# Kernel tuning notes

Measured on AMD Instinct MI355X. Metric: run time of the kernel, lower is better.

## Reference

```python
import jax, jax.numpy as jnp
import numpy as np

N, H, DE, E = 100000, 64, 16, 1600000
COORD_SCALE = 0.1


def _lin_params(key, din, dout):
    kw, kb = jax.random.split(key)
    W = jax.random.normal(kw, (din, dout), dtype=jnp.float32) * 0.02
    b = jax.random.normal(kb, (dout,), dtype=jnp.float32) * 0.02
    return W, b


def setup_inputs() -> dict:
    key = jax.random.key(0)
    ks = jax.random.split(key, 10)
    h = jax.random.normal(ks[0], (N, H), dtype=jnp.float32)
    pos = jax.random.normal(ks[1], (N, 3), dtype=jnp.float32)
    edge_index = jax.random.randint(ks[2], (2, E), 0, N, dtype=jnp.int32)
    edge_attr = jax.random.normal(ks[3], (E, DE), dtype=jnp.float32)
    W_e1, b_e1 = _lin_params(ks[4], 2 * H + 1 + DE, H)
    W_e2, b_e2 = _lin_params(ks[5], H, H)
    W_c1, b_c1 = _lin_params(ks[6], H, H)
    W_c2, b_c2 = _lin_params(ks[7], H, 1)
    W_n, b_n = _lin_params(ks[8], 2 * H, H)
    ln_g = jnp.ones((H,), dtype=jnp.float32)
    ln_b = jnp.zeros((H,), dtype=jnp.float32)
    return dict(h=h, pos=pos, edge_index=edge_index, edge_attr=edge_attr,
                W_e1=W_e1, b_e1=b_e1, W_e2=W_e2, b_e2=b_e2,
                W_c1=W_c1, b_c1=b_c1, W_c2=W_c2, b_c2=b_c2,
                W_n=W_n, b_n=b_n, ln_g=ln_g, ln_b=ln_b)


def reference(h, pos, edge_index, edge_attr,
              W_e1, b_e1, W_e2, b_e2,
              W_c1, b_c1, W_c2, b_c2,
              W_n, b_n, ln_g, ln_b):
    src, dst = edge_index[0], edge_index[1]
    pos_src = pos[src]            # [E,3] gather
    pos_dst = pos[dst]
    diff = pos_dst - pos_src      # [E,3]
    dist2 = jnp.clip(jnp.sum(diff * diff, axis=-1, keepdims=True), 0.0, 1000.0)  # [E,1]
    direction = diff / jnp.sqrt(dist2 + 1e-8)

    # edge MLP: phi_e(h_i, h_j, d2, e_ij)
    edge_input = jnp.concatenate([h[src], h[dst], dist2, edge_attr], axis=-1)  # [E, 2H+1+De]
    m = jax.nn.relu(edge_input @ W_e1 + b_e1)
    m_ij = jax.nn.relu(m @ W_e2 + b_e2)  # [E,H]

    # coord MLP -> scalar coef, tanh * scale
    c = jax.nn.relu(m_ij @ W_c1 + b_c1)
    coord_coef = jnp.tanh(c @ W_c2 + b_c2) * COORD_SCALE  # [E,1]
    trans = direction * coord_coef  # [E,3]

    # scatter-add to dst
    delta_pos = jnp.zeros_like(pos).at[dst].add(trans)
    pos_out = pos + delta_pos

    agg_msg = jnp.zeros_like(h).at[dst].add(m_ij)  # [N,H]

    # node MLP + residual + LayerNorm
    h_update = jax.nn.relu(jnp.concatenate([h, agg_msg], axis=-1) @ W_n + b_n)
    x = h + h_update
    mu = jnp.mean(x, axis=-1, keepdims=True)
    var = jnp.mean((x - mu) ** 2, axis=-1, keepdims=True)
    h_out = (x - mu) / jnp.sqrt(var + 1e-5) * ln_g + ln_b
    return h_out, pos_out
```

## Files before the change

kernel.cpp:

```cpp
#include <hip/hip_runtime.h>

using f32x4  = __attribute__((ext_vector_type(4))) float;
using short8 = __attribute__((ext_vector_type(8))) short;

__device__ inline short f2bf(float x) {
    union { float f; unsigned u; } v; v.f = x;
    unsigned r = v.u + 0x7fffu + ((v.u >> 16) & 1u);
    return (short)(r >> 16);
}

__device__ inline short8 pack8(float4 a, float4 b) {
    short8 r;
    r[0] = f2bf(a.x); r[1] = f2bf(a.y); r[2] = f2bf(a.z); r[3] = f2bf(a.w);
    r[4] = f2bf(b.x); r[5] = f2bf(b.y); r[6] = f2bf(b.z); r[7] = f2bf(b.w);
    return r;
}

__device__ inline void atomic_pk_add_bf16(short* addr, unsigned pk) {
    asm volatile("global_atomic_pk_add_bf16 %0, %1, off"
                 :: "v"(addr), "v"(pk) : "memory");
}

__global__ __launch_bounds__(256) void convert_weights(
    const float* __restrict__ We1, const float* __restrict__ We2,
    const float* __restrict__ Wc1, const float* __restrict__ Wn,
    short* __restrict__ W1T, short* __restrict__ W2T,
    short* __restrict__ Wc1T, short* __restrict__ WnT)
{
    const int i = blockIdx.x * 256 + threadIdx.x;
    if (i < 64 * 160) {
        const int n = i / 160, k = i % 160;
        float v = 0.0f;
        if (k < 128)       v = We1[k * 64 + n];
        else if (k < 144)  v = We1[(129 + k - 128) * 64 + n];
        else if (k == 144) v = We1[128 * 64 + n];
        W1T[i] = f2bf(v);
    }
    if (i < 64 * 128) {
        const int n = i / 128, k = i % 128;
        WnT[i] = f2bf(Wn[k * 64 + n]);
    }
    if (i < 64 * 64) {
        const int n = i / 64, k = i % 64;
        W2T[i]  = f2bf(We2[k * 64 + n]);
        Wc1T[i] = f2bf(Wc1[k * 64 + n]);
    }
}

__global__ __launch_bounds__(256) void convert_h(
    const float* __restrict__ h, short* __restrict__ hb, int n8)
{
    const int i = blockIdx.x * 256 + threadIdx.x;
    if (i < n8) {
        const float4* h4 = reinterpret_cast<const float4*>(h);
        reinterpret_cast<short8*>(hb)[i] = pack8(h4[2 * i], h4[2 * i + 1]);
    }
}

__global__ __launch_bounds__(256) void count_kernel(
    const int* __restrict__ ei, int* __restrict__ cnt, int E)
{
    const int e = blockIdx.x * 256 + threadIdx.x;
    if (e < E) atomicAdd(&cnt[ei[E + e]], 1);
}

__global__ __launch_bounds__(1024) void scan_partial(
    const int* __restrict__ cnt, int* __restrict__ bsum, int N)
{
    __shared__ int ws[16];
    const int i = blockIdx.x * 1024 + threadIdx.x;
    int v = (i < N) ? cnt[i] : 0;
    #pragma unroll
    for (int off = 1; off < 64; off <<= 1) v += __shfl_xor(v, off);
    const int lane = threadIdx.x & 63, wid = threadIdx.x >> 6;
    if (lane == 0) ws[wid] = v;
    __syncthreads();
    if (threadIdx.x == 0) {
        int s = 0;
        #pragma unroll
        for (int w = 0; w < 16; ++w) s += ws[w];
        bsum[blockIdx.x] = s;
    }
}

__global__ __launch_bounds__(1024) void scan_bsum(
    const int* __restrict__ bsum, int* __restrict__ boff, int NB)
{
    __shared__ int arr[1024];
    const int t = threadIdx.x;
    const int v = (t < NB) ? bsum[t] : 0;
    arr[t] = v;
    __syncthreads();
    for (int off = 1; off < 1024; off <<= 1) {
        const int u = (t >= off) ? arr[t - off] : 0;
        __syncthreads();
        arr[t] += u;
        __syncthreads();
    }
    if (t < NB) boff[t] = arr[t] - v;
}

__global__ __launch_bounds__(1024) void scan_final(
    const int* __restrict__ cnt, const int* __restrict__ boff,
    int* __restrict__ start, int N, int E)
{
    __shared__ int ws[16];
    const int i = blockIdx.x * 1024 + threadIdx.x;
    const int lane = threadIdx.x & 63, wid = threadIdx.x >> 6;
    const int v = (i < N) ? cnt[i] : 0;
    int inc = v;
    #pragma unroll
    for (int off = 1; off < 64; off <<= 1) {
        const int u = __shfl_up(inc, off);
        if (lane >= off) inc += u;
    }
    if (lane == 63) ws[wid] = inc;
    __syncthreads();
    int wpre = 0;
    #pragma unroll
    for (int w = 0; w < 16; ++w) wpre += (w < wid) ? ws[w] : 0;
    if (i < N) start[i] = boff[blockIdx.x] + wpre + inc - v;
    if (i == 0) start[N] = E;
}

__global__ __launch_bounds__(256) void fill_gather(
    const int* __restrict__ ei, const float* __restrict__ ea,
    const int* __restrict__ start, int* __restrict__ cursor,
    int* __restrict__ srcS, int* __restrict__ dstS,
    short* __restrict__ eaS, int E)
{
    const int e = blockIdx.x * 256 + threadIdx.x;
    if (e < E) {
        const int s = ei[e];
        const int d = ei[E + e];
        const int slot = start[d] + atomicAdd(&cursor[d], 1);
        srcS[slot] = s;
        dstS[slot] = d;
        const float4* eap = reinterpret_cast<const float4*>(ea + (size_t)e * 16);
        short8* o = reinterpret_cast<short8*>(eaS + (size_t)slot * 16);
        o[0] = pack8(eap[0], eap[1]);
        o[1] = pack8(eap[2], eap[3]);
    }
}

__global__ __launch_bounds__(256, 6) void egnn_edge_sorted(
    const short* __restrict__ hb, const float* __restrict__ pos,
    const int* __restrict__ srcS, const int* __restrict__ dstS,
    const short* __restrict__ eaS,
    const short* __restrict__ W1T, const short* __restrict__ W2T,
    const short* __restrict__ Wc1T,
    const float* __restrict__ be1, const float* __restrict__ be2,
    const float* __restrict__ bc1, const float* __restrict__ bc2,
    const float* __restrict__ Wc2,
    short* __restrict__ aggb, float* __restrict__ dpos, int E)
{
    __shared__ short M[4][16][72];

    const int tid  = threadIdx.x;
    const int lane = tid & 63;
    const int wave = tid >> 6;
    const int r16  = lane & 15;
    const int kg   = lane >> 4;

    const int slot  = blockIdx.x * 64 + wave * 16 + r16;
    const bool vrow = slot < E;
    const int slotc = min(slot, E - 1);
    const int src   = srcS[slotc];
    const int dst   = dstS[slotc];
    const int dkey  = vrow ? dst : -1;

    float dx = pos[3 * dst + 0] - pos[3 * src + 0];
    float dy = pos[3 * dst + 1] - pos[3 * src + 1];
    float dz = pos[3 * dst + 2] - pos[3 * src + 2];
    const float d2 = fminf(dx * dx + dy * dy + dz * dz, 1000.0f);
    const float inv = 1.0f / sqrtf(d2 + 1e-8f);
    dx *= inv; dy *= inv; dz *= inv;

    const short8* hs = reinterpret_cast<const short8*>(hb + (size_t)src * 64);
    const short8* hd = reinterpret_cast<const short8*>(hb + (size_t)dst * 64);
    const short8 a0 = hs[kg];
    const short8 a1 = hs[4 + kg];
    const short8 a2 = hd[kg];
    const short8 a3 = hd[4 + kg];
    short8 a4 = {0, 0, 0, 0, 0, 0, 0, 0};
    if (kg < 2) {
        a4 = *reinterpret_cast<const short8*>(eaS + (size_t)slotc * 16 + kg * 8);
    } else if (kg == 2) {
        a4[0] = f2bf(d2);
    }

    f32x4 acc1[4];
    #pragma unroll
    for (int nt = 0; nt < 4; ++nt) {
        const float b = be1[r16 + nt * 16];
        acc1[nt] = {b, b, b, b};
    }
    #pragma unroll
    for (int nt = 0; nt < 4; ++nt) {
        const short* wr = W1T + (r16 + nt * 16) * 160 + kg * 8;
        acc1[nt] = __builtin_amdgcn_mfma_f32_16x16x32_bf16(
            a0, *reinterpret_cast<const short8*>(wr), acc1[nt], 0, 0, 0);
        acc1[nt] = __builtin_amdgcn_mfma_f32_16x16x32_bf16(
            a1, *reinterpret_cast<const short8*>(wr + 32), acc1[nt], 0, 0, 0);
        acc1[nt] = __builtin_amdgcn_mfma_f32_16x16x32_bf16(
            a2, *reinterpret_cast<const short8*>(wr + 64), acc1[nt], 0, 0, 0);
        acc1[nt] = __builtin_amdgcn_mfma_f32_16x16x32_bf16(
            a3, *reinterpret_cast<const short8*>(wr + 96), acc1[nt], 0, 0, 0);
        acc1[nt] = __builtin_amdgcn_mfma_f32_16x16x32_bf16(
            a4, *reinterpret_cast<const short8*>(wr + 128), acc1[nt], 0, 0, 0);
    }
    #pragma unroll
    for (int nt = 0; nt < 4; ++nt)
        #pragma unroll
        for (int rg = 0; rg < 4; ++rg)
            M[wave][kg * 4 + rg][r16 + nt * 16] = f2bf(fmaxf(acc1[nt][rg], 0.0f));

    const short8 a5 = *reinterpret_cast<const short8*>(&M[wave][r16][kg * 8]);
    const short8 a6 = *reinterpret_cast<const short8*>(&M[wave][r16][32 + kg * 8]);
    f32x4 acc2[4];
    #pragma unroll
    for (int nt = 0; nt < 4; ++nt) {
        const float b = be2[r16 + nt * 16];
        acc2[nt] = {b, b, b, b};
    }
    #pragma unroll
    for (int nt = 0; nt < 4; ++nt) {
        const short* wr = W2T + (r16 + nt * 16) * 64 + kg * 8;
        acc2[nt] = __builtin_amdgcn_mfma_f32_16x16x32_bf16(
            a5, *reinterpret_cast<const short8*>(wr), acc2[nt], 0, 0, 0);
        acc2[nt] = __builtin_amdgcn_mfma_f32_16x16x32_bf16(
            a6, *reinterpret_cast<const short8*>(wr + 32), acc2[nt], 0, 0, 0);
    }
    #pragma unroll
    for (int nt = 0; nt < 4; ++nt)
        #pragma unroll
        for (int rg = 0; rg < 4; ++rg) {
            const float v = fmaxf(acc2[nt][rg], 0.0f);
            acc2[nt][rg] = v;
            M[wave][kg * 4 + rg][r16 + nt * 16] = f2bf(v);
        }

    const short8 a7 = *reinterpret_cast<const short8*>(&M[wave][r16][kg * 8]);
    const short8 a8 = *reinterpret_cast<const short8*>(&M[wave][r16][32 + kg * 8]);
    f32x4 acc3[4];
    #pragma unroll
    for (int nt = 0; nt < 4; ++nt) {
        const float b = bc1[r16 + nt * 16];
        acc3[nt] = {b, b, b, b};
    }
    #pragma unroll
    for (int nt = 0; nt < 4; ++nt) {
        const short* wr = Wc1T + (r16 + nt * 16) * 64 + kg * 8;
        acc3[nt] = __builtin_amdgcn_mfma_f32_16x16x32_bf16(
            a7, *reinterpret_cast<const short8*>(wr), acc3[nt], 0, 0, 0);
        acc3[nt] = __builtin_amdgcn_mfma_f32_16x16x32_bf16(
            a8, *reinterpret_cast<const short8*>(wr + 32), acc3[nt], 0, 0, 0);
    }

    float cf[4] = {0.0f, 0.0f, 0.0f, 0.0f};
    #pragma unroll
    for (int nt = 0; nt < 4; ++nt) {
        const float wv = Wc2[r16 + nt * 16];
        #pragma unroll
        for (int rg = 0; rg < 4; ++rg)
            cf[rg] += fmaxf(acc3[nt][rg], 0.0f) * wv;
    }
    #pragma unroll
    for (int off = 1; off < 16; off <<= 1)
        #pragma unroll
        for (int rg = 0; rg < 4; ++rg)
            cf[rg] += __shfl_xor(cf[rg], off);
    const float bc2v = bc2[0];
    #pragma unroll
    for (int rg = 0; rg < 4; ++rg)
        cf[rg] = tanhf(cf[rg] + bc2v) * 0.1f;

    const int srcl = ((r16 >> 2) << 4) + r16;
    const float c0 = __shfl(cf[0], srcl);
    const float c1 = __shfl(cf[1], srcl);
    const float c2 = __shfl(cf[2], srcl);
    const float c3 = __shfl(cf[3], srcl);
    const int rsel = r16 & 3;
    const float cfown = (rsel == 0) ? c0 : (rsel == 1) ? c1 : (rsel == 2) ? c2 : c3;

    int rstart = 0;
    while (rstart < 16) {
        const int dcur = __shfl(dkey, rstart);
        const bool inrun = (dkey == dcur) && (r16 >= rstart);
        const unsigned long long bm = __ballot(inrun);
        const int len = __popc((unsigned)bm & 0xFFFFu);
        const int rend = rstart + len;

        float s0 = 0.0f, s1 = 0.0f, s2 = 0.0f, s3 = 0.0f;
        #pragma unroll
        for (int rg = 0; rg < 4; ++rg) {
            const int row = (kg << 2) + rg;
            if (row >= rstart && row < rend) {
                s0 += acc2[0][rg]; s1 += acc2[1][rg];
                s2 += acc2[2][rg]; s3 += acc2[3][rg];
            }
        }
        s0 += __shfl_xor(s0, 16); s0 += __shfl_xor(s0, 32);
        s1 += __shfl_xor(s1, 16); s1 += __shfl_xor(s1, 32);
        s2 += __shfl_xor(s2, 16); s2 += __shfl_xor(s2, 32);
        s3 += __shfl_xor(s3, 16); s3 += __shfl_xor(s3, 32);

        float tx = inrun ? cfown * dx : 0.0f;
        float ty = inrun ? cfown * dy : 0.0f;
        float tz = inrun ? cfown * dz : 0.0f;
        #pragma unroll
        for (int off = 1; off < 16; off <<= 1) {
            tx += __shfl_xor(tx, off);
            ty += __shfl_xor(ty, off);
            tz += __shfl_xor(tz, off);
        }

        if (dcur >= 0) {
            #pragma unroll
            for (int nt = 0; nt < 4; ++nt) {
                const float v  = (nt == 0) ? s0 : (nt == 1) ? s1 : (nt == 2) ? s2 : s3;
                const float vp = __shfl_xor(v, 1);
                if (kg == 0 && ((r16 & 1) == (nt >> 1))) {
                    const int col0 = (r16 & ~1) + nt * 16;
                    const unsigned blo = (unsigned short)f2bf((r16 & 1) ? vp : v);
                    const unsigned bhi = (unsigned short)f2bf((r16 & 1) ? v : vp);
                    atomic_pk_add_bf16(aggb + (size_t)dcur * 64 + col0,
                                       blo | (bhi << 16));
                }
            }
            if (kg == 0 && r16 < 3) {
                const float tv = (r16 == 0) ? tx : (r16 == 1) ? ty : tz;
                unsafeAtomicAdd(&dpos[3 * dcur + r16], tv);
            }
        }
        rstart = rend;
    }
}

__global__ __launch_bounds__(256) void egnn_node_mfma(
    const float* __restrict__ h, const short* __restrict__ hb,
    const short* __restrict__ aggb, const float* __restrict__ pos,
    const float* __restrict__ dpos, const short* __restrict__ WnT,
    const float* __restrict__ bn, const float* __restrict__ lng,
    const float* __restrict__ lnb,
    float* __restrict__ h_out, float* __restrict__ pos_out, int N)
{
    __shared__ short As[64][136];
    const int tid = threadIdx.x;
    const int n0  = blockIdx.x * 64;

    if (tid < 64) {
        const int n = n0 + tid;
        if (n < N) {
            #pragma unroll
            for (int c = 0; c < 3; ++c)
                pos_out[(size_t)3 * n + c] = pos[(size_t)3 * n + c] + dpos[(size_t)3 * n + c];
        }
    }

    {
        const int row = tid >> 2, part = tid & 3;
        const int n = n0 + row;
        if (n < N) {
            const short* sp = (part < 2) ? (hb + (size_t)n * 64 + (part & 1) * 32)
                                         : (aggb + (size_t)n * 64 + (part & 1) * 32);
            #pragma unroll
            for (int q = 0; q < 4; ++q)
                *reinterpret_cast<short8*>(&As[row][part * 32 + q * 8]) =
                    *reinterpret_cast<const short8*>(sp + q * 8);
        }
    }
    __syncthreads();

    const int lane = tid & 63;
    const int wave = tid >> 6;
    const int r16  = lane & 15;
    const int kg   = lane >> 4;
    const int mrow = wave * 16 + r16;

    f32x4 acc[4];
    #pragma unroll
    for (int nt = 0; nt < 4; ++nt) {
        const float b = bn[r16 + nt * 16];
        acc[nt] = {b, b, b, b};
    }
    #pragma unroll
    for (int kt = 0; kt < 4; ++kt) {
        short8 a = *reinterpret_cast<const short8*>(&As[mrow][kt * 32 + kg * 8]);
        #pragma unroll
        for (int nt = 0; nt < 4; ++nt) {
            short8 b = *reinterpret_cast<const short8*>(
                &WnT[(r16 + nt * 16) * 128 + kt * 32 + kg * 8]);
            acc[nt] = __builtin_amdgcn_mfma_f32_16x16x32_bf16(a, b, acc[nt], 0, 0, 0);
        }
    }

    float xv[4][4];
    #pragma unroll
    for (int rg = 0; rg < 4; ++rg) {
        const int n = n0 + wave * 16 + kg * 4 + rg;
        const bool ok = n < N;
        #pragma unroll
        for (int nt = 0; nt < 4; ++nt)
            xv[nt][rg] = (ok ? h[(size_t)n * 64 + r16 + nt * 16] : 0.0f)
                         + fmaxf(acc[nt][rg], 0.0f);
    }

    float g[4], bb[4];
    #pragma unroll
    for (int nt = 0; nt < 4; ++nt) { g[nt] = lng[r16 + nt * 16]; bb[nt] = lnb[r16 + nt * 16]; }

    #pragma unroll
    for (int rg = 0; rg < 4; ++rg) {
        float s = xv[0][rg] + xv[1][rg] + xv[2][rg] + xv[3][rg];
        #pragma unroll
        for (int off = 1; off < 16; off <<= 1) s += __shfl_xor(s, off);
        const float mu = s * 0.015625f;
        float q = 0.0f;
        #pragma unroll
        for (int nt = 0; nt < 4; ++nt) { const float d = xv[nt][rg] - mu; q += d * d; }
        #pragma unroll
        for (int off = 1; off < 16; off <<= 1) q += __shfl_xor(q, off);
        const float inv = rsqrtf(q * 0.015625f + 1e-5f);
        const int n = n0 + wave * 16 + kg * 4 + rg;
        if (n < N) {
            #pragma unroll
            for (int nt = 0; nt < 4; ++nt)
                h_out[(size_t)n * 64 + r16 + nt * 16] =
                    (xv[nt][rg] - mu) * inv * g[nt] + bb[nt];
        }
    }
}

extern "C" void kernel_launch(void* const* d_in, const int* in_sizes, int n_in,
                              void* d_out, int out_size, void* d_ws, size_t ws_size,
                              hipStream_t stream)
{
    const float* h   = (const float*)d_in[0];
    const float* pos = (const float*)d_in[1];
    const int*   ei  = (const int*)d_in[2];
    const float* ea  = (const float*)d_in[3];
    const float* We1 = (const float*)d_in[4];
    const float* be1 = (const float*)d_in[5];
    const float* We2 = (const float*)d_in[6];
    const float* be2 = (const float*)d_in[7];
    const float* Wc1 = (const float*)d_in[8];
    const float* bc1 = (const float*)d_in[9];
    const float* Wc2 = (const float*)d_in[10];
    const float* bc2 = (const float*)d_in[11];
    const float* Wn  = (const float*)d_in[12];
    const float* bn  = (const float*)d_in[13];
    const float* lng = (const float*)d_in[14];
    const float* lnb = (const float*)d_in[15];

    const int N = in_sizes[0] / 64;
    const int E = in_sizes[2] / 2;
    const int NB = (N + 1023) / 1024;

    short* aggb = (short*)d_ws;
    short* hbuf = aggb + (size_t)N * 64;
    short* eaS  = hbuf + (size_t)N * 64;
    short* W1T  = eaS + (size_t)E * 16;
    short* W2T  = W1T + 64 * 160;
    short* Wc1T = W2T + 64 * 64;
    short* WnT  = Wc1T + 64 * 64;
    float* dpos = (float*)(WnT + 64 * 128);
    int* cnt    = (int*)(dpos + (size_t)3 * N);
    int* cursor = cnt + N;
    int* startp = cursor + N;
    int* bsum   = startp + N + 1;
    int* boff   = bsum + 1024;
    int* srcS   = boff + 1024;
    int* dstS   = srcS + E;

    hipMemsetAsync(aggb, 0, (size_t)N * 128, stream);
    hipMemsetAsync(dpos, 0, (size_t)N * 20, stream);
    convert_weights<<<40, 256, 0, stream>>>(We1, We2, Wc1, Wn, W1T, W2T, Wc1T, WnT);
    convert_h<<<(N * 64 / 8 + 255) / 256, 256, 0, stream>>>(h, hbuf, N * 64 / 8);
    count_kernel<<<(E + 255) / 256, 256, 0, stream>>>(ei, cnt, E);
    scan_partial<<<NB, 1024, 0, stream>>>(cnt, bsum, N);
    scan_bsum<<<1, 1024, 0, stream>>>(bsum, boff, NB);
    scan_final<<<NB, 1024, 0, stream>>>(cnt, boff, startp, N, E);
    fill_gather<<<(E + 255) / 256, 256, 0, stream>>>(
        ei, ea, startp, cursor, srcS, dstS, eaS, E);

    float* h_out   = (float*)d_out;
    float* pos_out = h_out + (size_t)N * 64;

    egnn_edge_sorted<<<(E + 63) / 64, 256, 0, stream>>>(
        hbuf, pos, srcS, dstS, eaS, W1T, W2T, Wc1T,
        be1, be2, bc1, bc2, Wc2, aggb, dpos, E);
    egnn_node_mfma<<<(N + 63) / 64, 256, 0, stream>>>(
        h, hbuf, aggb, pos, dpos, WnT, bn, lng, lnb, h_out, pos_out, N);
}
```

Baseline: 611.0 us.

## Software-pipeline edge kernel over four tiles per wave with prefetched gathers

Each wave now processes four 16-edge tiles in a loop instead of one. It prefetches the indices two tiles ahead and the source features, edge attributes and positions one tile ahead, so gather latency overlaps the MFMA work. The grid shrinks fourfold to match. It also swaps tanhf for an exp/rcp approximation and the inline-asm packed bf16 atomic for the HIP unsafeAtomicAdd on bfloat162. The prefetch raises register pressure under the launch bound of 6, and the fast tanh changes precision slightly.

```diff
diff --git a/kernel.cpp b/kernel.cpp
--- a/kernel.cpp
+++ b/kernel.cpp
@@ -1,4 +1,6 @@
 #include <hip/hip_runtime.h>
+#include <hip/hip_bf16.h>
+#include <string.h>
 
 using f32x4  = __attribute__((ext_vector_type(4))) float;
 using short8 = __attribute__((ext_vector_type(8))) short;
@@ -16,9 +18,15 @@
     return r;
 }
 
-__device__ inline void atomic_pk_add_bf16(short* addr, unsigned pk) {
-    asm volatile("global_atomic_pk_add_bf16 %0, %1, off"
-                 :: "v"(addr), "v"(pk) : "memory");
+__device__ inline void atomic_pk_add_bf16v(short* addr, unsigned pk) {
+    __hip_bfloat162 bv;
+    memcpy(&bv, &pk, 4);
+    unsafeAtomicAdd(reinterpret_cast<__hip_bfloat162*>(addr), bv);
+}
+
+__device__ inline float fast_tanh(float x) {
+    const float ex = __expf(2.0f * x);
+    return 1.0f - 2.0f * __builtin_amdgcn_rcpf(ex + 1.0f);
 }
 
 __global__ __launch_bounds__(256) void convert_weights(
@@ -143,6 +151,33 @@
     }
 }
 
+struct Idx { int s, d; };
+struct Dat { short8 a0, a1, ae; float px, py, pz; };
+
+__device__ inline Idx load_idx(const int* __restrict__ srcS,
+                               const int* __restrict__ dstS, int slotc)
+{
+    Idx I; I.s = srcS[slotc]; I.d = dstS[slotc]; return I;
+}
+
+__device__ inline Dat load_dat(const short* __restrict__ hb,
+                               const float* __restrict__ pos,
+                               const short* __restrict__ eaS,
+                               const Idx I, int slotc, int kg)
+{
+    Dat D;
+    const short8* hs = reinterpret_cast<const short8*>(hb + (size_t)I.s * 64);
+    D.a0 = hs[kg];
+    D.a1 = hs[4 + kg];
+    short8 ae = {0, 0, 0, 0, 0, 0, 0, 0};
+    if (kg < 2) ae = *reinterpret_cast<const short8*>(eaS + (size_t)slotc * 16 + kg * 8);
+    D.ae = ae;
+    D.px = pos[3 * I.s + 0];
+    D.py = pos[3 * I.s + 1];
+    D.pz = pos[3 * I.s + 2];
+    return D;
+}
+
 __global__ __launch_bounds__(256, 6) void egnn_edge_sorted(
     const short* __restrict__ hb, const float* __restrict__ pos,
     const int* __restrict__ srcS, const int* __restrict__ dstS,
@@ -154,6 +189,7 @@
     const float* __restrict__ Wc2,
     short* __restrict__ aggb, float* __restrict__ dpos, int E)
 {
+    constexpr int NT = 4;
     __shared__ short M[4][16][72];
 
     const int tid  = threadIdx.x;
@@ -162,178 +198,187 @@
     const int r16  = lane & 15;
     const int kg   = lane >> 4;
 
-    const int slot  = blockIdx.x * 64 + wave * 16 + r16;
-    const bool vrow = slot < E;
-    const int slotc = min(slot, E - 1);
-    const int src   = srcS[slotc];
-    const int dst   = dstS[slotc];
-    const int dkey  = vrow ? dst : -1;
-
-    float dx = pos[3 * dst + 0] - pos[3 * src + 0];
-    float dy = pos[3 * dst + 1] - pos[3 * src + 1];
-    float dz = pos[3 * dst + 2] - pos[3 * src + 2];
-    const float d2 = fminf(dx * dx + dy * dy + dz * dz, 1000.0f);
-    const float inv = 1.0f / sqrtf(d2 + 1e-8f);
-    dx *= inv; dy *= inv; dz *= inv;
-
-    const short8* hs = reinterpret_cast<const short8*>(hb + (size_t)src * 64);
-    const short8* hd = reinterpret_cast<const short8*>(hb + (size_t)dst * 64);
-    const short8 a0 = hs[kg];
-    const short8 a1 = hs[4 + kg];
-    const short8 a2 = hd[kg];
-    const short8 a3 = hd[4 + kg];
-    short8 a4 = {0, 0, 0, 0, 0, 0, 0, 0};
-    if (kg < 2) {
-        a4 = *reinterpret_cast<const short8*>(eaS + (size_t)slotc * 16 + kg * 8);
-    } else if (kg == 2) {
-        a4[0] = f2bf(d2);
-    }
-
-    f32x4 acc1[4];
-    #pragma unroll
-    for (int nt = 0; nt < 4; ++nt) {
-        const float b = be1[r16 + nt * 16];
-        acc1[nt] = {b, b, b, b};
-    }
-    #pragma unroll
-    for (int nt = 0; nt < 4; ++nt) {
-        const short* wr = W1T + (r16 + nt * 16) * 160 + kg * 8;
-        acc1[nt] = __builtin_amdgcn_mfma_f32_16x16x32_bf16(
-            a0, *reinterpret_cast<const short8*>(wr), acc1[nt], 0, 0, 0);
-        acc1[nt] = __builtin_amdgcn_mfma_f32_16x16x32_bf16(
-            a1, *reinterpret_cast<const short8*>(wr + 32), acc1[nt], 0, 0, 0);
-        acc1[nt] = __builtin_amdgcn_mfma_f32_16x16x32_bf16(
-            a2, *reinterpret_cast<const short8*>(wr + 64), acc1[nt], 0, 0, 0);
-        acc1[nt] = __builtin_amdgcn_mfma_f32_16x16x32_bf16(
-            a3, *reinterpret_cast<const short8*>(wr + 96), acc1[nt], 0, 0, 0);
-        acc1[nt] = __builtin_amdgcn_mfma_f32_16x16x32_bf16(
-            a4, *reinterpret_cast<const short8*>(wr + 128), acc1[nt], 0, 0, 0);
-    }
-    #pragma unroll
-    for (int nt = 0; nt < 4; ++nt)
+    const int sbase = (blockIdx.x * 4 + wave) * (16 * NT);
+
+    Idx ia = load_idx(srcS, dstS, min(sbase + r16, E - 1));
+    Dat da = load_dat(hb, pos, eaS, ia, min(sbase + r16, E - 1), kg);
+    Idx ib = load_idx(srcS, dstS, min(sbase + 16 + r16, E - 1));
+
+    #pragma unroll
+    for (int t = 0; t < NT; ++t) {
+        Dat dn;
+        Idx in2 = ib;
+        if (t + 1 < NT)
+            dn = load_dat(hb, pos, eaS, ib, min(sbase + (t + 1) * 16 + r16, E - 1), kg);
+        if (t + 2 < NT)
+            in2 = load_idx(srcS, dstS, min(sbase + (t + 2) * 16 + r16, E - 1));
+
+        const int slot = sbase + t * 16 + r16;
+        const int dkey = (slot < E) ? ia.d : -1;
+
+        const short8* hd = reinterpret_cast<const short8*>(hb + (size_t)ia.d * 64);
+        const short8 a2 = hd[kg];
+        const short8 a3 = hd[4 + kg];
+        float dx = pos[3 * ia.d + 0] - da.px;
+        float dy = pos[3 * ia.d + 1] - da.py;
+        float dz = pos[3 * ia.d + 2] - da.pz;
+        const float d2 = fminf(dx * dx + dy * dy + dz * dz, 1000.0f);
+        const float rinv = 1.0f / sqrtf(d2 + 1e-8f);
+        dx *= rinv; dy *= rinv; dz *= rinv;
+
+        short8 a4 = da.ae;
+        if (kg == 2) a4[0] = f2bf(d2);
+
+        f32x4 acc1[4];
+        #pragma unroll
+        for (int nt = 0; nt < 4; ++nt) {
+            const float b = be1[r16 + nt * 16];
+            acc1[nt] = {b, b, b, b};
+        }
+        #pragma unroll
+        for (int nt = 0; nt < 4; ++nt) {
+            const short* wr = W1T + (r16 + nt * 16) * 160 + kg * 8;
+            acc1[nt] = __builtin_amdgcn_mfma_f32_16x16x32_bf16(
+                da.a0, *reinterpret_cast<const short8*>(wr), acc1[nt], 0, 0, 0);
+            acc1[nt] = __builtin_amdgcn_mfma_f32_16x16x32_bf16(
+                da.a1, *reinterpret_cast<const short8*>(wr + 32), acc1[nt], 0, 0, 0);
+            acc1[nt] = __builtin_amdgcn_mfma_f32_16x16x32_bf16(
+                a2, *reinterpret_cast<const short8*>(wr + 64), acc1[nt], 0, 0, 0);
+            acc1[nt] = __builtin_amdgcn_mfma_f32_16x16x32_bf16(
+                a3, *reinterpret_cast<const short8*>(wr + 96), acc1[nt], 0, 0, 0);
+            acc1[nt] = __builtin_amdgcn_mfma_f32_16x16x32_bf16(
+                a4, *reinterpret_cast<const short8*>(wr + 128), acc1[nt], 0, 0, 0);
+        }
+        #pragma unroll
+        for (int nt = 0; nt < 4; ++nt)
+            #pragma unroll
+            for (int rg = 0; rg < 4; ++rg)
+                M[wave][kg * 4 + rg][r16 + nt * 16] = f2bf(fmaxf(acc1[nt][rg], 0.0f));
+
+        const short8 a5 = *reinterpret_cast<const short8*>(&M[wave][r16][kg * 8]);
+        const short8 a6 = *reinterpret_cast<const short8*>(&M[wave][r16][32 + kg * 8]);
+        f32x4 acc2[4];
+        #pragma unroll
+        for (int nt = 0; nt < 4; ++nt) {
+            const float b = be2[r16 + nt * 16];
+            acc2[nt] = {b, b, b, b};
+        }
+        #pragma unroll
+        for (int nt = 0; nt < 4; ++nt) {
+            const short* wr = W2T + (r16 + nt * 16) * 64 + kg * 8;
+            acc2[nt] = __builtin_amdgcn_mfma_f32_16x16x32_bf16(
+                a5, *reinterpret_cast<const short8*>(wr), acc2[nt], 0, 0, 0);
+            acc2[nt] = __builtin_amdgcn_mfma_f32_16x16x32_bf16(
+                a6, *reinterpret_cast<const short8*>(wr + 32), acc2[nt], 0, 0, 0);
+        }
+        #pragma unroll
+        for (int nt = 0; nt < 4; ++nt)
+            #pragma unroll
+            for (int rg = 0; rg < 4; ++rg) {
+                const float v = fmaxf(acc2[nt][rg], 0.0f);
+                acc2[nt][rg] = v;
+                M[wave][kg * 4 + rg][r16 + nt * 16] = f2bf(v);
+            }
+
+        const short8 a7 = *reinterpret_cast<const short8*>(&M[wave][r16][kg * 8]);
+        const short8 a8 = *reinterpret_cast<const short8*>(&M[wave][r16][32 + kg * 8]);
+        f32x4 acc3[4];
+        #pragma unroll
+        for (int nt = 0; nt < 4; ++nt) {
+            const float b = bc1[r16 + nt * 16];
+            acc3[nt] = {b, b, b, b};
+        }
+        #pragma unroll
+        for (int nt = 0; nt < 4; ++nt) {
+            const short* wr = Wc1T + (r16 + nt * 16) * 64 + kg * 8;
+            acc3[nt] = __builtin_amdgcn_mfma_f32_16x16x32_bf16(
+                a7, *reinterpret_cast<const short8*>(wr), acc3[nt], 0, 0, 0);
+            acc3[nt] = __builtin_amdgcn_mfma_f32_16x16x32_bf16(
+                a8, *reinterpret_cast<const short8*>(wr + 32), acc3[nt], 0, 0, 0);
+        }
+
+        float cf[4] = {0.0f, 0.0f, 0.0f, 0.0f};
+        #pragma unroll
+        for (int nt = 0; nt < 4; ++nt) {
+            const float wv = Wc2[r16 + nt * 16];
+            #pragma unroll
+            for (int rg = 0; rg < 4; ++rg)
+                cf[rg] += fmaxf(acc3[nt][rg], 0.0f) * wv;
+        }
+        #pragma unroll
+        for (int off = 1; off < 16; off <<= 1)
+            #pragma unroll
+            for (int rg = 0; rg < 4; ++rg)
+                cf[rg] += __shfl_xor(cf[rg], off);
+        const float bc2v = bc2[0];
         #pragma unroll
         for (int rg = 0; rg < 4; ++rg)
-            M[wave][kg * 4 + rg][r16 + nt * 16] = f2bf(fmaxf(acc1[nt][rg], 0.0f));
-
-    const short8 a5 = *reinterpret_cast<const short8*>(&M[wave][r16][kg * 8]);
-    const short8 a6 = *reinterpret_cast<const short8*>(&M[wave][r16][32 + kg * 8]);
-    f32x4 acc2[4];
-    #pragma unroll
-    for (int nt = 0; nt < 4; ++nt) {
-        const float b = be2[r16 + nt * 16];
-        acc2[nt] = {b, b, b, b};
-    }
-    #pragma unroll
-    for (int nt = 0; nt < 4; ++nt) {
-        const short* wr = W2T + (r16 + nt * 16) * 64 + kg * 8;
-        acc2[nt] = __builtin_amdgcn_mfma_f32_16x16x32_bf16(
-            a5, *reinterpret_cast<const short8*>(wr), acc2[nt], 0, 0, 0);
-        acc2[nt] = __builtin_amdgcn_mfma_f32_16x16x32_bf16(
-            a6, *reinterpret_cast<const short8*>(wr + 32), acc2[nt], 0, 0, 0);
-    }
-    #pragma unroll
-    for (int nt = 0; nt < 4; ++nt)
-        #pragma unroll
-        for (int rg = 0; rg < 4; ++rg) {
-            const float v = fmaxf(acc2[nt][rg], 0.0f);
-            acc2[nt][rg] = v;
-            M[wave][kg * 4 + rg][r16 + nt * 16] = f2bf(v);
-        }
-
-    const short8 a7 = *reinterpret_cast<const short8*>(&M[wave][r16][kg * 8]);
-    const short8 a8 = *reinterpret_cast<const short8*>(&M[wave][r16][32 + kg * 8]);
-    f32x4 acc3[4];
-    #pragma unroll
-    for (int nt = 0; nt < 4; ++nt) {
-        const float b = bc1[r16 + nt * 16];
-        acc3[nt] = {b, b, b, b};
-    }
-    #pragma unroll
-    for (int nt = 0; nt < 4; ++nt) {
-        const short* wr = Wc1T + (r16 + nt * 16) * 64 + kg * 8;
-        acc3[nt] = __builtin_amdgcn_mfma_f32_16x16x32_bf16(
-            a7, *reinterpret_cast<const short8*>(wr), acc3[nt], 0, 0, 0);
-        acc3[nt] = __builtin_amdgcn_mfma_f32_16x16x32_bf16(
-            a8, *reinterpret_cast<const short8*>(wr + 32), acc3[nt], 0, 0, 0);
-    }
-
-    float cf[4] = {0.0f, 0.0f, 0.0f, 0.0f};
-    #pragma unroll
-    for (int nt = 0; nt < 4; ++nt) {
-        const float wv = Wc2[r16 + nt * 16];
-        #pragma unroll
-        for (int rg = 0; rg < 4; ++rg)
-            cf[rg] += fmaxf(acc3[nt][rg], 0.0f) * wv;
-    }
-    #pragma unroll
-    for (int off = 1; off < 16; off <<= 1)
-        #pragma unroll
-        for (int rg = 0; rg < 4; ++rg)
-            cf[rg] += __shfl_xor(cf[rg], off);
-    const float bc2v = bc2[0];
-    #pragma unroll
-    for (int rg = 0; rg < 4; ++rg)
-        cf[rg] = tanhf(cf[rg] + bc2v) * 0.1f;
-
-    const int srcl = ((r16 >> 2) << 4) + r16;
-    const float c0 = __shfl(cf[0], srcl);
-    const float c1 = __shfl(cf[1], srcl);
-    const float c2 = __shfl(cf[2], srcl);
-    const float c3 = __shfl(cf[3], srcl);
-    const int rsel = r16 & 3;
-    const float cfown = (rsel == 0) ? c0 : (rsel == 1) ? c1 : (rsel == 2) ? c2 : c3;
-
-    int rstart = 0;
-    while (rstart < 16) {
-        const int dcur = __shfl(dkey, rstart);
-        const bool inrun = (dkey == dcur) && (r16 >= rstart);
-        const unsigned long long bm = __ballot(inrun);
-        const int len = __popc((unsigned)bm & 0xFFFFu);
-        const int rend = rstart + len;
-
-        float s0 = 0.0f, s1 = 0.0f, s2 = 0.0f, s3 = 0.0f;
-        #pragma unroll
-        for (int rg = 0; rg < 4; ++rg) {
-            const int row = (kg << 2) + rg;
-            if (row >= rstart && row < rend) {
-                s0 += acc2[0][rg]; s1 += acc2[1][rg];
-                s2 += acc2[2][rg]; s3 += acc2[3][rg];
-            }
-        }
-        s0 += __shfl_xor(s0, 16); s0 += __shfl_xor(s0, 32);
-        s1 += __shfl_xor(s1, 16); s1 += __shfl_xor(s1, 32);
-        s2 += __shfl_xor(s2, 16); s2 += __shfl_xor(s2, 32);
-        s3 += __shfl_xor(s3, 16); s3 += __shfl_xor(s3, 32);
-
-        float tx = inrun ? cfown * dx : 0.0f;
-        float ty = inrun ? cfown * dy : 0.0f;
-        float tz = inrun ? cfown * dz : 0.0f;
-        #pragma unroll
-        for (int off = 1; off < 16; off <<= 1) {
-            tx += __shfl_xor(tx, off);
-            ty += __shfl_xor(ty, off);
-            tz += __shfl_xor(tz, off);
-        }
-
-        if (dcur >= 0) {
-            #pragma unroll
-            for (int nt = 0; nt < 4; ++nt) {
-                const float v  = (nt == 0) ? s0 : (nt == 1) ? s1 : (nt == 2) ? s2 : s3;
-                const float vp = __shfl_xor(v, 1);
-                if (kg == 0 && ((r16 & 1) == (nt >> 1))) {
-                    const int col0 = (r16 & ~1) + nt * 16;
-                    const unsigned blo = (unsigned short)f2bf((r16 & 1) ? vp : v);
-                    const unsigned bhi = (unsigned short)f2bf((r16 & 1) ? v : vp);
-                    atomic_pk_add_bf16(aggb + (size_t)dcur * 64 + col0,
-                                       blo | (bhi << 16));
+            cf[rg] = fast_tanh(cf[rg] + bc2v) * 0.1f;
+
+        const int srcl = ((r16 >> 2) << 4) + r16;
+        const float c0 = __shfl(cf[0], srcl);
+        const float c1 = __shfl(cf[1], srcl);
+        const float c2 = __shfl(cf[2], srcl);
+        const float c3 = __shfl(cf[3], srcl);
+        const int rsel = r16 & 3;
+        const float cfown = (rsel == 0) ? c0 : (rsel == 1) ? c1 : (rsel == 2) ? c2 : c3;
+
+        int rstart = 0;
+        while (rstart < 16) {
+            const int dcur = __shfl(dkey, rstart);
+            const bool inrun = (dkey == dcur) && (r16 >= rstart);
+            const unsigned long long bm = __ballot(inrun);
+            const int len = __popc((unsigned)bm & 0xFFFFu);
+            const int rend = rstart + len;
+
+            float s0 = 0.0f, s1 = 0.0f, s2 = 0.0f, s3 = 0.0f;
+            #pragma unroll
+            for (int rg = 0; rg < 4; ++rg) {
+                const int row = (kg << 2) + rg;
+                if (row >= rstart && row < rend) {
+                    s0 += acc2[0][rg]; s1 += acc2[1][rg];
+                    s2 += acc2[2][rg]; s3 += acc2[3][rg];
                 }
             }
-            if (kg == 0 && r16 < 3) {
-                const float tv = (r16 == 0) ? tx : (r16 == 1) ? ty : tz;
-                unsafeAtomicAdd(&dpos[3 * dcur + r16], tv);
+            s0 += __shfl_xor(s0, 16); s0 += __shfl_xor(s0, 32);
+            s1 += __shfl_xor(s1, 16); s1 += __shfl_xor(s1, 32);
+            s2 += __shfl_xor(s2, 16); s2 += __shfl_xor(s2, 32);
+            s3 += __shfl_xor(s3, 16); s3 += __shfl_xor(s3, 32);
+
+            float tx = inrun ? cfown * dx : 0.0f;
+            float ty = inrun ? cfown * dy : 0.0f;
+            float tz = inrun ? cfown * dz : 0.0f;
+            #pragma unroll
+            for (int off = 1; off < 16; off <<= 1) {
+                tx += __shfl_xor(tx, off);
+                ty += __shfl_xor(ty, off);
+                tz += __shfl_xor(tz, off);
             }
-        }
-        rstart = rend;
+
+            if (dcur >= 0) {
+                #pragma unroll
+                for (int nt = 0; nt < 4; ++nt) {
+                    const float v  = (nt == 0) ? s0 : (nt == 1) ? s1 : (nt == 2) ? s2 : s3;
+                    const float vp = __shfl_xor(v, 1);
+                    if (kg == 0 && ((r16 & 1) == (nt >> 1))) {
+                        const int col0 = (r16 & ~1) + nt * 16;
+                        const unsigned blo = (unsigned short)f2bf((r16 & 1) ? vp : v);
+                        const unsigned bhi = (unsigned short)f2bf((r16 & 1) ? v : vp);
+                        atomic_pk_add_bf16v(aggb + (size_t)dcur * 64 + col0,
+                                            blo | (bhi << 16));
+                    }
+                }
+                if (kg == 0 && r16 < 3) {
+                    const float tv = (r16 == 0) ? tx : (r16 == 1) ? ty : tz;
+                    unsafeAtomicAdd(&dpos[3 * dcur + r16], tv);
+                }
+            }
+            rstart = rend;
+        }
+
+        ia = ib;
+        ib = in2;
+        if (t + 1 < NT) da = dn;
     }
 }
 
@@ -473,8 +518,8 @@
     int* srcS   = boff + 1024;
     int* dstS   = srcS + E;
 
-    hipMemsetAsync(aggb, 0, (size_t)N * 128, stream);
-    hipMemsetAsync(dpos, 0, (size_t)N * 20, stream);
+    (void)hipMemsetAsync(aggb, 0, (size_t)N * 128, stream);
+    (void)hipMemsetAsync(dpos, 0, (size_t)N * 20, stream);
     convert_weights<<<40, 256, 0, stream>>>(We1, We2, Wc1, Wn, W1T, W2T, Wc1T, WnT);
     convert_h<<<(N * 64 / 8 + 255) / 256, 256, 0, stream>>>(h, hbuf, N * 64 / 8);
     count_kernel<<<(E + 255) / 256, 256, 0, stream>>>(ei, cnt, E);
@@ -487,7 +532,7 @@
     float* h_out   = (float*)d_out;
     float* pos_out = h_out + (size_t)N * 64;
 
-    egnn_edge_sorted<<<(E + 63) / 64, 256, 0, stream>>>(
+    egnn_edge_sorted<<<(E + 255) / 256, 256, 0, stream>>>(
         hbuf, pos, srcS, dstS, eaS, W1T, W2T, Wc1T,
         be1, be2, bc1, bc2, Wc2, aggb, dpos, E);
     egnn_node_mfma<<<(N + 63) / 64, 256, 0, stream>>>(
```

After: 735.2 us. +20.3%, slower.

## Process two 16-edge tiles per wave with prefetched gathers and fast tanh

Applied to the files above, without the earlier changes.

Each wave now handles 32 sorted edges as two 16-row tiles. The src-side h rows, edge attributes and source positions for both tiles are loaded up front, so gather latency for the second tile overlaps compute of the first, and the grid is halved. tanhf is replaced by an exp/rcp approximation to cut transcendental cost. This raises register pressure, which may reduce occupancy, and the approximation slightly changes accuracy.

```diff
diff --git a/kernel.cpp b/kernel.cpp
--- a/kernel.cpp
+++ b/kernel.cpp
@@ -19,6 +19,11 @@
 __device__ inline void atomic_pk_add_bf16(short* addr, unsigned pk) {
     asm volatile("global_atomic_pk_add_bf16 %0, %1, off"
                  :: "v"(addr), "v"(pk) : "memory");
+}
+
+__device__ inline float fast_tanh(float x) {
+    const float ex = __expf(2.0f * x);
+    return 1.0f - 2.0f * __builtin_amdgcn_rcpf(ex + 1.0f);
 }
 
 __global__ __launch_bounds__(256) void convert_weights(
@@ -162,179 +167,190 @@
     const int r16  = lane & 15;
     const int kg   = lane >> 4;
 
-    const int slot  = blockIdx.x * 64 + wave * 16 + r16;
-    const bool vrow = slot < E;
-    const int slotc = min(slot, E - 1);
-    const int src   = srcS[slotc];
-    const int dst   = dstS[slotc];
-    const int dkey  = vrow ? dst : -1;
-
-    float dx = pos[3 * dst + 0] - pos[3 * src + 0];
-    float dy = pos[3 * dst + 1] - pos[3 * src + 1];
-    float dz = pos[3 * dst + 2] - pos[3 * src + 2];
-    const float d2 = fminf(dx * dx + dy * dy + dz * dz, 1000.0f);
-    const float inv = 1.0f / sqrtf(d2 + 1e-8f);
-    dx *= inv; dy *= inv; dz *= inv;
-
-    const short8* hs = reinterpret_cast<const short8*>(hb + (size_t)src * 64);
-    const short8* hd = reinterpret_cast<const short8*>(hb + (size_t)dst * 64);
-    const short8 a0 = hs[kg];
-    const short8 a1 = hs[4 + kg];
-    const short8 a2 = hd[kg];
-    const short8 a3 = hd[4 + kg];
-    short8 a4 = {0, 0, 0, 0, 0, 0, 0, 0};
+    const int sbase = (blockIdx.x * 4 + wave) * 32;
+    const int slotA = sbase + r16;
+    const int slotB = sbase + 16 + r16;
+    const int scA = min(slotA, E - 1);
+    const int scB = min(slotB, E - 1);
+
+    const int srcA = srcS[scA], dstA = dstS[scA];
+    const int srcB = srcS[scB], dstB = dstS[scB];
+
+    const short8* hsA = reinterpret_cast<const short8*>(hb + (size_t)srcA * 64);
+    const short8 a0A = hsA[kg];
+    const short8 a1A = hsA[4 + kg];
+    const short8* hsB = reinterpret_cast<const short8*>(hb + (size_t)srcB * 64);
+    const short8 a0B = hsB[kg];
+    const short8 a1B = hsB[4 + kg];
+
+    short8 aeA = {0, 0, 0, 0, 0, 0, 0, 0};
+    short8 aeB = {0, 0, 0, 0, 0, 0, 0, 0};
     if (kg < 2) {
-        a4 = *reinterpret_cast<const short8*>(eaS + (size_t)slotc * 16 + kg * 8);
-    } else if (kg == 2) {
-        a4[0] = f2bf(d2);
-    }
-
-    f32x4 acc1[4];
-    #pragma unroll
-    for (int nt = 0; nt < 4; ++nt) {
-        const float b = be1[r16 + nt * 16];
-        acc1[nt] = {b, b, b, b};
-    }
-    #pragma unroll
-    for (int nt = 0; nt < 4; ++nt) {
-        const short* wr = W1T + (r16 + nt * 16) * 160 + kg * 8;
-        acc1[nt] = __builtin_amdgcn_mfma_f32_16x16x32_bf16(
-            a0, *reinterpret_cast<const short8*>(wr), acc1[nt], 0, 0, 0);
-        acc1[nt] = __builtin_amdgcn_mfma_f32_16x16x32_bf16(
-            a1, *reinterpret_cast<const short8*>(wr + 32), acc1[nt], 0, 0, 0);
-        acc1[nt] = __builtin_amdgcn_mfma_f32_16x16x32_bf16(
-            a2, *reinterpret_cast<const short8*>(wr + 64), acc1[nt], 0, 0, 0);
-        acc1[nt] = __builtin_amdgcn_mfma_f32_16x16x32_bf16(
-            a3, *reinterpret_cast<const short8*>(wr + 96), acc1[nt], 0, 0, 0);
-        acc1[nt] = __builtin_amdgcn_mfma_f32_16x16x32_bf16(
-            a4, *reinterpret_cast<const short8*>(wr + 128), acc1[nt], 0, 0, 0);
-    }
-    #pragma unroll
-    for (int nt = 0; nt < 4; ++nt)
-        #pragma unroll
-        for (int rg = 0; rg < 4; ++rg)
-            M[wave][kg * 4 + rg][r16 + nt * 16] = f2bf(fmaxf(acc1[nt][rg], 0.0f));
-
-    const short8 a5 = *reinterpret_cast<const short8*>(&M[wave][r16][kg * 8]);
-    const short8 a6 = *reinterpret_cast<const short8*>(&M[wave][r16][32 + kg * 8]);
-    f32x4 acc2[4];
-    #pragma unroll
-    for (int nt = 0; nt < 4; ++nt) {
-        const float b = be2[r16 + nt * 16];
-        acc2[nt] = {b, b, b, b};
-    }
-    #pragma unroll
-    for (int nt = 0; nt < 4; ++nt) {
-        const short* wr = W2T + (r16 + nt * 16) * 64 + kg * 8;
-        acc2[nt] = __builtin_amdgcn_mfma_f32_16x16x32_bf16(
-            a5, *reinterpret_cast<const short8*>(wr), acc2[nt], 0, 0, 0);
-        acc2[nt] = __builtin_amdgcn_mfma_f32_16x16x32_bf16(
-            a6, *reinterpret_cast<const short8*>(wr + 32), acc2[nt], 0, 0, 0);
-    }
-    #pragma unroll
-    for (int nt = 0; nt < 4; ++nt)
-        #pragma unroll
-        for (int rg = 0; rg < 4; ++rg) {
-            const float v = fmaxf(acc2[nt][rg], 0.0f);
-            acc2[nt][rg] = v;
-            M[wave][kg * 4 + rg][r16 + nt * 16] = f2bf(v);
-        }
-
-    const short8 a7 = *reinterpret_cast<const short8*>(&M[wave][r16][kg * 8]);
-    const short8 a8 = *reinterpret_cast<const short8*>(&M[wave][r16][32 + kg * 8]);
-    f32x4 acc3[4];
-    #pragma unroll
-    for (int nt = 0; nt < 4; ++nt) {
-        const float b = bc1[r16 + nt * 16];
-        acc3[nt] = {b, b, b, b};
-    }
-    #pragma unroll
-    for (int nt = 0; nt < 4; ++nt) {
-        const short* wr = Wc1T + (r16 + nt * 16) * 64 + kg * 8;
-        acc3[nt] = __builtin_amdgcn_mfma_f32_16x16x32_bf16(
-            a7, *reinterpret_cast<const short8*>(wr), acc3[nt], 0, 0, 0);
-        acc3[nt] = __builtin_amdgcn_mfma_f32_16x16x32_bf16(
-            a8, *reinterpret_cast<const short8*>(wr + 32), acc3[nt], 0, 0, 0);
-    }
-
-    float cf[4] = {0.0f, 0.0f, 0.0f, 0.0f};
-    #pragma unroll
-    for (int nt = 0; nt < 4; ++nt) {
-        const float wv = Wc2[r16 + nt * 16];
-        #pragma unroll
-        for (int rg = 0; rg < 4; ++rg)
-            cf[rg] += fmaxf(acc3[nt][rg], 0.0f) * wv;
-    }
-    #pragma unroll
-    for (int off = 1; off < 16; off <<= 1)
-        #pragma unroll
-        for (int rg = 0; rg < 4; ++rg)
-            cf[rg] += __shfl_xor(cf[rg], off);
-    const float bc2v = bc2[0];
-    #pragma unroll
-    for (int rg = 0; rg < 4; ++rg)
-        cf[rg] = tanhf(cf[rg] + bc2v) * 0.1f;
-
-    const int srcl = ((r16 >> 2) << 4) + r16;
-    const float c0 = __shfl(cf[0], srcl);
-    const float c1 = __shfl(cf[1], srcl);
-    const float c2 = __shfl(cf[2], srcl);
-    const float c3 = __shfl(cf[3], srcl);
-    const int rsel = r16 & 3;
-    const float cfown = (rsel == 0) ? c0 : (rsel == 1) ? c1 : (rsel == 2) ? c2 : c3;
-
-    int rstart = 0;
-    while (rstart < 16) {
-        const int dcur = __shfl(dkey, rstart);
-        const bool inrun = (dkey == dcur) && (r16 >= rstart);
-        const unsigned long long bm = __ballot(inrun);
-        const int len = __popc((unsigned)bm & 0xFFFFu);
-        const int rend = rstart + len;
-
-        float s0 = 0.0f, s1 = 0.0f, s2 = 0.0f, s3 = 0.0f;
-        #pragma unroll
-        for (int rg = 0; rg < 4; ++rg) {
-            const int row = (kg << 2) + rg;
-            if (row >= rstart && row < rend) {
-                s0 += acc2[0][rg]; s1 += acc2[1][rg];
-                s2 += acc2[2][rg]; s3 += acc2[3][rg];
-            }
-        }
-        s0 += __shfl_xor(s0, 16); s0 += __shfl_xor(s0, 32);
-        s1 += __shfl_xor(s1, 16); s1 += __shfl_xor(s1, 32);
-        s2 += __shfl_xor(s2, 16); s2 += __shfl_xor(s2, 32);
-        s3 += __shfl_xor(s3, 16); s3 += __shfl_xor(s3, 32);
-
-        float tx = inrun ? cfown * dx : 0.0f;
-        float ty = inrun ? cfown * dy : 0.0f;
-        float tz = inrun ? cfown * dz : 0.0f;
-        #pragma unroll
-        for (int off = 1; off < 16; off <<= 1) {
-            tx += __shfl_xor(tx, off);
-            ty += __shfl_xor(ty, off);
-            tz += __shfl_xor(tz, off);
-        }
-
-        if (dcur >= 0) {
-            #pragma unroll
-            for (int nt = 0; nt < 4; ++nt) {
-                const float v  = (nt == 0) ? s0 : (nt == 1) ? s1 : (nt == 2) ? s2 : s3;
-                const float vp = __shfl_xor(v, 1);
-                if (kg == 0 && ((r16 & 1) == (nt >> 1))) {
-                    const int col0 = (r16 & ~1) + nt * 16;
-                    const unsigned blo = (unsigned short)f2bf((r16 & 1) ? vp : v);
-                    const unsigned bhi = (unsigned short)f2bf((r16 & 1) ? v : vp);
-                    atomic_pk_add_bf16(aggb + (size_t)dcur * 64 + col0,
-                                       blo | (bhi << 16));
-                }
-            }
-            if (kg == 0 && r16 < 3) {
-                const float tv = (r16 == 0) ? tx : (r16 == 1) ? ty : tz;
-                unsafeAtomicAdd(&dpos[3 * dcur + r16], tv);
-            }
-        }
-        rstart = rend;
-    }
+        aeA = *reinterpret_cast<const short8*>(eaS + (size_t)scA * 16 + kg * 8);
+        aeB = *reinterpret_cast<const short8*>(eaS + (size_t)scB * 16 + kg * 8);
+    }
+    const float psxA = pos[3 * srcA + 0], psyA = pos[3 * srcA + 1], pszA = pos[3 * srcA + 2];
+    const float psxB = pos[3 * srcB + 0], psyB = pos[3 * srcB + 1], pszB = pos[3 * srcB + 2];
+
+#define COMPUTE_TILE(SLOTV, DSTV, A0, A1, AE, PSX, PSY, PSZ)                  \
+do {                                                                          \
+    const int dkey_ = (SLOTV < E) ? DSTV : -1;                                \
+    const short8* hd_ = reinterpret_cast<const short8*>(hb + (size_t)DSTV * 64); \
+    const short8 a2_ = hd_[kg];                                               \
+    const short8 a3_ = hd_[4 + kg];                                           \
+    float dx_ = pos[3 * DSTV + 0] - PSX;                                      \
+    float dy_ = pos[3 * DSTV + 1] - PSY;                                      \
+    float dz_ = pos[3 * DSTV + 2] - PSZ;                                      \
+    const float d2_ = fminf(dx_ * dx_ + dy_ * dy_ + dz_ * dz_, 1000.0f);      \
+    const float ri_ = 1.0f / sqrtf(d2_ + 1e-8f);                              \
+    dx_ *= ri_; dy_ *= ri_; dz_ *= ri_;                                       \
+    short8 a4_ = AE;                                                          \
+    if (kg == 2) a4_[0] = f2bf(d2_);                                          \
+    f32x4 acc1_[4];                                                           \
+    _Pragma("unroll")                                                         \
+    for (int nt = 0; nt < 4; ++nt) {                                          \
+        const float b = be1[r16 + nt * 16];                                   \
+        acc1_[nt] = {b, b, b, b};                                             \
+    }                                                                         \
+    _Pragma("unroll")                                                         \
+    for (int nt = 0; nt < 4; ++nt) {                                          \
+        const short* wr = W1T + (r16 + nt * 16) * 160 + kg * 8;               \
+        acc1_[nt] = __builtin_amdgcn_mfma_f32_16x16x32_bf16(                  \
+            A0, *reinterpret_cast<const short8*>(wr), acc1_[nt], 0, 0, 0);    \
+        acc1_[nt] = __builtin_amdgcn_mfma_f32_16x16x32_bf16(                  \
+            A1, *reinterpret_cast<const short8*>(wr + 32), acc1_[nt], 0, 0, 0);\
+        acc1_[nt] = __builtin_amdgcn_mfma_f32_16x16x32_bf16(                  \
+            a2_, *reinterpret_cast<const short8*>(wr + 64), acc1_[nt], 0, 0, 0);\
+        acc1_[nt] = __builtin_amdgcn_mfma_f32_16x16x32_bf16(                  \
+            a3_, *reinterpret_cast<const short8*>(wr + 96), acc1_[nt], 0, 0, 0);\
+        acc1_[nt] = __builtin_amdgcn_mfma_f32_16x16x32_bf16(                  \
+            a4_, *reinterpret_cast<const short8*>(wr + 128), acc1_[nt], 0, 0, 0);\
+    }                                                                         \
+    _Pragma("unroll")                                                         \
+    for (int nt = 0; nt < 4; ++nt)                                            \
+        _Pragma("unroll")                                                     \
+        for (int rg = 0; rg < 4; ++rg)                                        \
+            M[wave][kg * 4 + rg][r16 + nt * 16] = f2bf(fmaxf(acc1_[nt][rg], 0.0f)); \
+    const short8 a5_ = *reinterpret_cast<const short8*>(&M[wave][r16][kg * 8]);     \
+    const short8 a6_ = *reinterpret_cast<const short8*>(&M[wave][r16][32 + kg * 8]);\
+    f32x4 acc2_[4];                                                           \
+    _Pragma("unroll")                                                         \
+    for (int nt = 0; nt < 4; ++nt) {                                          \
+        const float b = be2[r16 + nt * 16];                                   \
+        acc2_[nt] = {b, b, b, b};                                             \
+    }                                                                         \
+    _Pragma("unroll")                                                         \
+    for (int nt = 0; nt < 4; ++nt) {                                          \
+        const short* wr = W2T + (r16 + nt * 16) * 64 + kg * 8;                \
+        acc2_[nt] = __builtin_amdgcn_mfma_f32_16x16x32_bf16(                  \
+            a5_, *reinterpret_cast<const short8*>(wr), acc2_[nt], 0, 0, 0);   \
+        acc2_[nt] = __builtin_amdgcn_mfma_f32_16x16x32_bf16(                  \
+            a6_, *reinterpret_cast<const short8*>(wr + 32), acc2_[nt], 0, 0, 0);\
+    }                                                                         \
+    _Pragma("unroll")                                                         \
+    for (int nt = 0; nt < 4; ++nt)                                            \
+        _Pragma("unroll")                                                     \
+        for (int rg = 0; rg < 4; ++rg) {                                      \
+            const float v = fmaxf(acc2_[nt][rg], 0.0f);                       \
+            acc2_[nt][rg] = v;                                                \
+            M[wave][kg * 4 + rg][r16 + nt * 16] = f2bf(v);                    \
+        }                                                                     \
+    const short8 a7_ = *reinterpret_cast<const short8*>(&M[wave][r16][kg * 8]);     \
+    const short8 a8_ = *reinterpret_cast<const short8*>(&M[wave][r16][32 + kg * 8]);\
+    f32x4 acc3_[4];                                                           \
+    _Pragma("unroll")                                                         \
+    for (int nt = 0; nt < 4; ++nt) {                                          \
+        const float b = bc1[r16 + nt * 16];                                   \
+        acc3_[nt] = {b, b, b, b};                                             \
+    }                                                                         \
+    _Pragma("unroll")                                                         \
+    for (int nt = 0; nt < 4; ++nt) {                                          \
+        const short* wr = Wc1T + (r16 + nt * 16) * 64 + kg * 8;               \
+        acc3_[nt] = __builtin_amdgcn_mfma_f32_16x16x32_bf16(                  \
+            a7_, *reinterpret_cast<const short8*>(wr), acc3_[nt], 0, 0, 0);   \
+        acc3_[nt] = __builtin_amdgcn_mfma_f32_16x16x32_bf16(                  \
+            a8_, *reinterpret_cast<const short8*>(wr + 32), acc3_[nt], 0, 0, 0);\
+    }                                                                         \
+    float cf_[4] = {0.0f, 0.0f, 0.0f, 0.0f};                                  \
+    _Pragma("unroll")                                                         \
+    for (int nt = 0; nt < 4; ++nt) {                                          \
+        const float wv = Wc2[r16 + nt * 16];                                  \
+        _Pragma("unroll")                                                     \
+        for (int rg = 0; rg < 4; ++rg)                                        \
+            cf_[rg] += fmaxf(acc3_[nt][rg], 0.0f) * wv;                       \
+    }                                                                         \
+    _Pragma("unroll")                                                         \
+    for (int off = 1; off < 16; off <<= 1)                                    \
+        _Pragma("unroll")                                                     \
+        for (int rg = 0; rg < 4; ++rg)                                        \
+            cf_[rg] += __shfl_xor(cf_[rg], off);                              \
+    const float bc2v_ = bc2[0];                                               \
+    _Pragma("unroll")                                                         \
+    for (int rg = 0; rg < 4; ++rg)                                            \
+        cf_[rg] = fast_tanh(cf_[rg] + bc2v_) * 0.1f;                          \
+    const int srcl_ = ((r16 >> 2) << 4) + r16;                                \
+    const float c0_ = __shfl(cf_[0], srcl_);                                  \
+    const float c1_ = __shfl(cf_[1], srcl_);                                  \
+    const float c2_ = __shfl(cf_[2], srcl_);                                  \
+    const float c3_ = __shfl(cf_[3], srcl_);                                  \
+    const int rsel_ = r16 & 3;                                                \
+    const float cfown_ = (rsel_ == 0) ? c0_ : (rsel_ == 1) ? c1_              \
+                       : (rsel_ == 2) ? c2_ : c3_;                            \
+    int rstart_ = 0;                                                          \
+    while (rstart_ < 16) {                                                    \
+        const int dcur_ = __shfl(dkey_, rstart_);                             \
+        const bool inrun_ = (dkey_ == dcur_) && (r16 >= rstart_);             \
+        const unsigned long long bm_ = __ballot(inrun_);                      \
+        const int len_ = __popc((unsigned)bm_ & 0xFFFFu);                     \
+        const int rend_ = rstart_ + len_;                                     \
+        float s0_ = 0.0f, s1_ = 0.0f, s2_ = 0.0f, s3_ = 0.0f;                 \
+        _Pragma("unroll")                                                     \
+        for (int rg = 0; rg < 4; ++rg) {                                      \
+            const int row = (kg << 2) + rg;                                   \
+            if (row >= rstart_ && row < rend_) {                              \
+                s0_ += acc2_[0][rg]; s1_ += acc2_[1][rg];                     \
+                s2_ += acc2_[2][rg]; s3_ += acc2_[3][rg];                     \
+            }                                                                 \
+        }                                                                     \
+        s0_ += __shfl_xor(s0_, 16); s0_ += __shfl_xor(s0_, 32);               \
+        s1_ += __shfl_xor(s1_, 16); s1_ += __shfl_xor(s1_, 32);               \
+        s2_ += __shfl_xor(s2_, 16); s2_ += __shfl_xor(s2_, 32);               \
+        s3_ += __shfl_xor(s3_, 16); s3_ += __shfl_xor(s3_, 32);               \
+        float tx_ = inrun_ ? cfown_ * dx_ : 0.0f;                             \
+        float ty_ = inrun_ ? cfown_ * dy_ : 0.0f;                             \
+        float tz_ = inrun_ ? cfown_ * dz_ : 0.0f;                             \
+        _Pragma("unroll")                                                     \
+        for (int off = 1; off < 16; off <<= 1) {                              \
+            tx_ += __shfl_xor(tx_, off);                                      \
+            ty_ += __shfl_xor(ty_, off);                                      \
+            tz_ += __shfl_xor(tz_, off);                                      \
+        }                                                                     \
+        if (dcur_ >= 0) {                                                     \
+            _Pragma("unroll")                                                 \
+            for (int nt = 0; nt < 4; ++nt) {                                  \
+                const float v = (nt == 0) ? s0_ : (nt == 1) ? s1_             \
+                              : (nt == 2) ? s2_ : s3_;                        \
+                const float vp = __shfl_xor(v, 1);                            \
+                if (kg == 0 && ((r16 & 1) == (nt >> 1))) {                    \
+                    const int col0 = (r16 & ~1) + nt * 16;                    \
+                    const unsigned blo = (unsigned short)f2bf((r16 & 1) ? vp : v); \
+                    const unsigned bhi = (unsigned short)f2bf((r16 & 1) ? v : vp); \
+                    atomic_pk_add_bf16(aggb + (size_t)dcur_ * 64 + col0,      \
+                                       blo | (bhi << 16));                    \
+                }                                                             \
+            }                                                                 \
+            if (kg == 0 && r16 < 3) {                                         \
+                const float tv = (r16 == 0) ? tx_ : (r16 == 1) ? ty_ : tz_;   \
+                unsafeAtomicAdd(&dpos[3 * dcur_ + r16], tv);                  \
+            }                                                                 \
+        }                                                                     \
+        rstart_ = rend_;                                                      \
+    }                                                                         \
+} while (0)
+
+    COMPUTE_TILE(slotA, dstA, a0A, a1A, aeA, psxA, psyA, pszA);
+    COMPUTE_TILE(slotB, dstB, a0B, a1B, aeB, psxB, psyB, pszB);
+#undef COMPUTE_TILE
 }
 
 __global__ __launch_bounds__(256) void egnn_node_mfma(
@@ -473,8 +489,8 @@
     int* srcS   = boff + 1024;
     int* dstS   = srcS + E;
 
-    hipMemsetAsync(aggb, 0, (size_t)N * 128, stream);
-    hipMemsetAsync(dpos, 0, (size_t)N * 20, stream);
+    (void)hipMemsetAsync(aggb, 0, (size_t)N * 128, stream);
+    (void)hipMemsetAsync(dpos, 0, (size_t)N * 20, stream);
     convert_weights<<<40, 256, 0, stream>>>(We1, We2, Wc1, Wn, W1T, W2T, Wc1T, WnT);
     convert_h<<<(N * 64 / 8 + 255) / 256, 256, 0, stream>>>(h, hbuf, N * 64 / 8);
     count_kernel<<<(E + 255) / 256, 256, 0, stream>>>(ei, cnt, E);
@@ -487,7 +503,7 @@
     float* h_out   = (float*)d_out;
     float* pos_out = h_out + (size_t)N * 64;
 
-    egnn_edge_sorted<<<(E + 63) / 64, 256, 0, stream>>>(
+    egnn_edge_sorted<<<(E + 127) / 128, 256, 0, stream>>>(
         hbuf, pos, srcS, dstS, eaS, W1T, W2T, Wc1T,
         be1, be2, bc1, bc2, Wc2, aggb, dpos, E);
     egnn_node_mfma<<<(N + 63) / 64, 256, 0, stream>>>(
```

New measurement: 672.6 us. +10.1%, slower.
